# Performance work log

Hardware: AMD Instinct MI355X
Metric: run time of the kernel (lower is better)

The kernel has to match this reference:

```python
import jax, jax.numpy as jnp
import numpy as np

B, D, H = 8192, 256, 512


def setup_inputs() -> dict:
    key = jax.random.key(0)
    ks = jax.random.split(key, 25)
    inp = {
        "x": jax.random.normal(ks[0], (B, D), jnp.float32),
        "h_t": jax.random.normal(ks[1], (B, H), jnp.float32),
        "h_s": jax.random.normal(ks[2], (B, H), jnp.float32),
        "c_t": jax.random.normal(ks[3], (B, H), jnp.float32),
        "c_s": jax.random.normal(ks[4], (B, H), jnp.float32),
    }
    names = ["Ui", "Wti", "Wsi", "bi", "Us", "Wts", "Wss", "bs",
             "Ut", "Wtt", "Wst", "bt", "Uo", "Wto", "Wso", "bo",
             "Uc", "Wtc", "Wsc", "bc"]
    shapes = {"U": (D, H), "W": (H, H), "b": (H,)}
    scale = 0.02  # keep activations in a sane range
    for i, n in enumerate(names):
        s = shapes["U"] if n[0] == "U" else (shapes["b"] if n[0] == "b" else shapes["W"])
        inp[n] = jax.random.normal(ks[5 + i], s, jnp.float32) * scale
    return inp


def reference(x, h_t, h_s, c_t, c_s,
              Ui, Wti, Wsi, bi, Us, Wts, Wss, bs,
              Ut, Wtt, Wst, bt, Uo, Wto, Wso, bo,
              Uc, Wtc, Wsc, bc):
    # Fuse the 15 small GEMMs into 3 concatenated GEMMs: [B,D]@[D,5H] etc.
    U = jnp.concatenate([Ui, Us, Ut, Uo, Uc], axis=1)      # [D, 5H]
    Wt = jnp.concatenate([Wti, Wts, Wtt, Wto, Wtc], axis=1)  # [H, 5H]
    Ws = jnp.concatenate([Wsi, Wss, Wst, Wso, Wsc], axis=1)  # [H, 5H]
    b = jnp.concatenate([bi, bs, bt, bo, bc])                # [5H]
    gates = x @ U + h_t @ Wt + h_s @ Ws + b                  # [B, 5H]
    g_i, g_fs, g_ft, g_o, g_c = jnp.split(gates, 5, axis=1)
    i_n = jax.nn.sigmoid(g_i)
    f_s_n = jax.nn.sigmoid(g_fs)
    f_t_n = jax.nn.sigmoid(g_ft)
    o_n = jax.nn.sigmoid(g_o)
    c_n = jnp.tanh(g_c)
    c_h = i_n * c_n + f_t_n * c_t + f_s_n * c_s
    h = o_n * jnp.tanh(c_h)
    return (h, c_h)
```

## Files before the change

### kernel.cpp

```cpp
#include <hip/hip_runtime.h>
#include <hip/hip_bf16.h>
#include <cstdint>
#include <cstddef>

#define B_  8192
#define D_  256
#define H_  512
#define K_  1280
#define N_  2560
#define NT_ 160

typedef short short8 __attribute__((ext_vector_type(8)));
typedef float f32x4  __attribute__((ext_vector_type(4)));

__device__ __forceinline__ float sigf(float x)     { return 1.f / (1.f + __expf(-x)); }
__device__ __forceinline__ float tanhfast(float x) { return 1.f - 2.f / (__expf(2.f * x) + 1.f); }

__global__ void convA_kernel(const float* __restrict__ x, const float* __restrict__ ht,
                             const float* __restrict__ hs, __hip_bfloat16* __restrict__ A) {
    int t = blockIdx.x * 256 + threadIdx.x;
    int idx8 = t * 8;
    int b = idx8 / K_;
    int k = idx8 - b * K_;
    const float* src;
    if (k < D_)            src = x  + (size_t)b * D_ + k;
    else if (k < D_ + H_)  src = ht + (size_t)b * H_ + (k - D_);
    else                   src = hs + (size_t)b * H_ + (k - D_ - H_);
    f32x4 v0 = *(const f32x4*)(src);
    f32x4 v1 = *(const f32x4*)(src + 4);
    union { short8 s; __hip_bfloat16 h[8]; } o;
    o.h[0] = __float2bfloat16(v0[0]); o.h[1] = __float2bfloat16(v0[1]);
    o.h[2] = __float2bfloat16(v0[2]); o.h[3] = __float2bfloat16(v0[3]);
    o.h[4] = __float2bfloat16(v1[0]); o.h[5] = __float2bfloat16(v1[1]);
    o.h[6] = __float2bfloat16(v1[2]); o.h[7] = __float2bfloat16(v1[3]);
    *(short8*)(A + idx8) = o.s;
}

struct WPtrs {
    const float* U[5];
    const float* Wt[5];
    const float* Ws[5];
};

__global__ void convW_kernel(WPtrs p, __hip_bfloat16* __restrict__ WT) {
    __shared__ __hip_bfloat16 tile[64][72];
    int g  = blockIdx.z;
    int k0 = blockIdx.y * 64;
    int h0 = blockIdx.x * 64;
    const float* src; int kl0;
    if (k0 < 256)      { src = p.U[g];  kl0 = k0; }
    else if (k0 < 768) { src = p.Wt[g]; kl0 = k0 - 256; }
    else               { src = p.Ws[g]; kl0 = k0 - 768; }
    int tid = threadIdx.x;
    int tk = tid >> 6;
    int th = tid & 63;
    for (int r = 0; r < 16; ++r) {
        int kl = r * 4 + tk;
        tile[kl][th] = __float2bfloat16(src[(size_t)(kl0 + kl) * H_ + h0 + th]);
    }
    __syncthreads();
    for (int r = 0; r < 16; ++r) {
        int hl = r * 4 + tk;
        int h  = h0 + hl;
        int np = (h >> 4) * 80 + g * 16 + (h & 15);
        WT[(size_t)np * K_ + k0 + th] = tile[th][hl];
    }
}

#define GLD16(gp, lp)                                                              \
    __builtin_amdgcn_global_load_lds(                                              \
        (const __attribute__((address_space(1))) unsigned int*)(gp),               \
        (__attribute__((address_space(3))) unsigned int*)(lp), 16, 0, 0)

__global__ __launch_bounds__(256) void gemm_fused_kernel(
    const __hip_bfloat16* __restrict__ A, const __hip_bfloat16* __restrict__ WT,
    const float* __restrict__ ct, const float* __restrict__ cs,
    const float* __restrict__ bi, const float* __restrict__ bfs,
    const float* __restrict__ bft, const float* __restrict__ bo,
    const float* __restrict__ bc, float* __restrict__ out) {
    __shared__ alignas(16) unsigned short sA[128 * 32];
    __shared__ alignas(16) unsigned short sB[NT_ * 32];

    int tid = threadIdx.x;
    int m0 = blockIdx.y * 128;
    int n0 = blockIdx.x * NT_;
    int wid  = tid >> 6, lane = tid & 63;
    int wm   = wid >> 1, wn   = wid & 1;
    int quad = lane >> 4, l15 = lane & 15;

    int h = (blockIdx.x * 2 + wn) * 16 + l15;
    float Bi = bi[h], Bfs = bfs[h], Bft = bft[h], Bo = bo[h], Bc = bc[h];

    f32x4 acc[4][5];
    for (int i = 0; i < 4; ++i)
        for (int j = 0; j < 5; ++j)
            acc[i][j] = (f32x4){0.f, 0.f, 0.f, 0.f};

    int srow = tid >> 2;
    int scol = (tid & 3) * 8;
    const __hip_bfloat16* Abase = A  + (size_t)(m0 + srow) * K_ + scol;
    const __hip_bfloat16* Bbase = WT + (size_t)(n0 + srow) * K_ + scol;
    unsigned short* AsDst = sA + tid * 8;
    unsigned short* BsDst = sB + tid * 8;

    for (int k0 = 0; k0 < K_; k0 += 32) {
        GLD16(Abase + k0,                    AsDst);
        GLD16(Abase + k0 + (size_t)64 * K_,  AsDst + 2048);
        GLD16(Bbase + k0,                    BsDst);
        GLD16(Bbase + k0 + (size_t)64 * K_,  BsDst + 2048);
        if (tid < 128)
            GLD16(Bbase + k0 + (size_t)128 * K_, BsDst + 4096);
        __syncthreads();

        short8 a[4], b[5];
        for (int f = 0; f < 4; ++f)
            a[f] = *(const short8*)(sA + (wm * 64 + f * 16 + l15) * 32 + quad * 8);
        for (int j = 0; j < 5; ++j)
            b[j] = *(const short8*)(sB + (wn * 80 + j * 16 + l15) * 32 + quad * 8);
        for (int i = 0; i < 4; ++i)
            for (int j = 0; j < 5; ++j)
                acc[i][j] = __builtin_amdgcn_mfma_f32_16x16x32_bf16(a[i], b[j], acc[i][j], 0, 0, 0);
        __syncthreads();
    }

    for (int i = 0; i < 4; ++i) {
        int row0 = m0 + wm * 64 + i * 16 + quad * 4;
        for (int r = 0; r < 4; ++r) {
            size_t idx = (size_t)(row0 + r) * H_ + h;
            float i_n  = sigf(acc[i][0][r] + Bi);
            float fs_n = sigf(acc[i][1][r] + Bfs);
            float ft_n = sigf(acc[i][2][r] + Bft);
            float o_n  = sigf(acc[i][3][r] + Bo);
            float c_n  = tanhfast(acc[i][4][r] + Bc);
            float ch   = i_n * c_n + ft_n * ct[idx] + fs_n * cs[idx];
            out[idx] = o_n * tanhfast(ch);
            out[(size_t)B_ * H_ + idx] = ch;
        }
    }
}

struct AllW {
    const float* U[5];
    const float* Wt[5];
    const float* Ws[5];
    const float* bias[5];
};

__global__ __launch_bounds__(512) void fallback_kernel(const float* __restrict__ x,
                                                       const float* __restrict__ ht,
                                                       const float* __restrict__ hs,
                                                       const float* __restrict__ ct,
                                                       const float* __restrict__ cs,
                                                       AllW w, float* __restrict__ out) {
    __shared__ float arow[K_];
    int b = blockIdx.x;
    int h = threadIdx.x;
    for (int k = h; k < K_; k += 512) {
        float v;
        if (k < D_)           v = x[b * D_ + k];
        else if (k < D_ + H_) v = ht[b * H_ + k - D_];
        else                  v = hs[b * H_ + k - D_ - H_];
        arow[k] = v;
    }
    __syncthreads();
    float g[5];
    for (int gi = 0; gi < 5; ++gi) {
        float s = w.bias[gi][h];
        const float* U = w.U[gi];
        for (int k = 0; k < D_; ++k) s += arow[k] * U[(size_t)k * H_ + h];
        const float* Wt = w.Wt[gi];
        for (int k = 0; k < H_; ++k) s += arow[D_ + k] * Wt[(size_t)k * H_ + h];
        const float* Ws = w.Ws[gi];
        for (int k = 0; k < H_; ++k) s += arow[D_ + H_ + k] * Ws[(size_t)k * H_ + h];
        g[gi] = s;
    }
    int idx = b * H_ + h;
    float i_n = sigf(g[0]), fs_n = sigf(g[1]), ft_n = sigf(g[2]), o_n = sigf(g[3]);
    float c_n = tanhfast(g[4]);
    float ch  = i_n * c_n + ft_n * ct[idx] + fs_n * cs[idx];
    out[idx] = o_n * tanhfast(ch);
    out[(size_t)B_ * H_ + idx] = ch;
}

extern "C" void kernel_launch(void* const* d_in, const int* in_sizes, int n_in,
                              void* d_out, int out_size, void* d_ws, size_t ws_size,
                              hipStream_t stream) {
    const float* x  = (const float*)d_in[0];
    const float* ht = (const float*)d_in[1];
    const float* hs = (const float*)d_in[2];
    const float* ct = (const float*)d_in[3];
    const float* cs = (const float*)d_in[4];

    WPtrs wp;
    AllW  aw;
    const float* bias[5];
    for (int g = 0; g < 5; ++g) {
        wp.U[g]  = (const float*)d_in[5 + g * 4 + 0];
        wp.Wt[g] = (const float*)d_in[5 + g * 4 + 1];
        wp.Ws[g] = (const float*)d_in[5 + g * 4 + 2];
        bias[g]  = (const float*)d_in[5 + g * 4 + 3];
        aw.U[g] = wp.U[g]; aw.Wt[g] = wp.Wt[g]; aw.Ws[g] = wp.Ws[g]; aw.bias[g] = bias[g];
    }
    float* out = (float*)d_out;

    size_t szA = (size_t)B_ * K_ * 2;
    size_t szW = (size_t)N_ * K_ * 2;

    if (ws_size >= szA + szW) {
        __hip_bfloat16* Abf = (__hip_bfloat16*)d_ws;
        __hip_bfloat16* WT  = (__hip_bfloat16*)((char*)d_ws + szA);

        convA_kernel<<<(B_ * K_ / 8) / 256, 256, 0, stream>>>(x, ht, hs, Abf);
        convW_kernel<<<dim3(8, 20, 5), 256, 0, stream>>>(wp, WT);
        gemm_fused_kernel<<<dim3(N_ / NT_, B_ / 128), 256, 0, stream>>>(
            Abf, WT, ct, cs, bias[0], bias[1], bias[2], bias[3], bias[4], out);
    } else {
        fallback_kernel<<<B_, 512, 0, stream>>>(x, ht, hs, ct, cs, aw, out);
    }
}
```

Baseline: 248.2 us.

## Merge prep kernels and use 8-wave GEMM blocks with smaller per-wave tiles

The two conversion kernels become one launch, where a block-index range selects either activation conversion or weight transpose. The GEMM block grows from 4 to 8 waves, each computing a 32x80 tile instead of 64x80. This halves accumulator registers per wave and should allow more waves per CU for latency hiding. The grid is also transposed so that consecutive blocks walk along M, which changes L2 reuse of the weight tiles, and the loops are explicitly unrolled. In exchange, each wave does fewer MFMAs per LDS read of B, and each block now needs 512 threads to fill its tile.

```diff
diff --git a/kernel.cpp b/kernel.cpp
--- a/kernel.cpp
+++ b/kernel.cpp
@@ -16,54 +16,59 @@
 __device__ __forceinline__ float sigf(float x)     { return 1.f / (1.f + __expf(-x)); }
 __device__ __forceinline__ float tanhfast(float x) { return 1.f - 2.f / (__expf(2.f * x) + 1.f); }
 
-__global__ void convA_kernel(const float* __restrict__ x, const float* __restrict__ ht,
-                             const float* __restrict__ hs, __hip_bfloat16* __restrict__ A) {
-    int t = blockIdx.x * 256 + threadIdx.x;
-    int idx8 = t * 8;
-    int b = idx8 / K_;
-    int k = idx8 - b * K_;
-    const float* src;
-    if (k < D_)            src = x  + (size_t)b * D_ + k;
-    else if (k < D_ + H_)  src = ht + (size_t)b * H_ + (k - D_);
-    else                   src = hs + (size_t)b * H_ + (k - D_ - H_);
-    f32x4 v0 = *(const f32x4*)(src);
-    f32x4 v1 = *(const f32x4*)(src + 4);
-    union { short8 s; __hip_bfloat16 h[8]; } o;
-    o.h[0] = __float2bfloat16(v0[0]); o.h[1] = __float2bfloat16(v0[1]);
-    o.h[2] = __float2bfloat16(v0[2]); o.h[3] = __float2bfloat16(v0[3]);
-    o.h[4] = __float2bfloat16(v1[0]); o.h[5] = __float2bfloat16(v1[1]);
-    o.h[6] = __float2bfloat16(v1[2]); o.h[7] = __float2bfloat16(v1[3]);
-    *(short8*)(A + idx8) = o.s;
-}
-
 struct WPtrs {
     const float* U[5];
     const float* Wt[5];
     const float* Ws[5];
 };
 
-__global__ void convW_kernel(WPtrs p, __hip_bfloat16* __restrict__ WT) {
+__global__ void prep_kernel(const float* __restrict__ x, const float* __restrict__ ht,
+                            const float* __restrict__ hs, WPtrs p,
+                            __hip_bfloat16* __restrict__ A, __hip_bfloat16* __restrict__ WT) {
     __shared__ __hip_bfloat16 tile[64][72];
-    int g  = blockIdx.z;
-    int k0 = blockIdx.y * 64;
-    int h0 = blockIdx.x * 64;
-    const float* src; int kl0;
-    if (k0 < 256)      { src = p.U[g];  kl0 = k0; }
-    else if (k0 < 768) { src = p.Wt[g]; kl0 = k0 - 256; }
-    else               { src = p.Ws[g]; kl0 = k0 - 768; }
-    int tid = threadIdx.x;
-    int tk = tid >> 6;
-    int th = tid & 63;
-    for (int r = 0; r < 16; ++r) {
-        int kl = r * 4 + tk;
-        tile[kl][th] = __float2bfloat16(src[(size_t)(kl0 + kl) * H_ + h0 + th]);
-    }
-    __syncthreads();
-    for (int r = 0; r < 16; ++r) {
-        int hl = r * 4 + tk;
-        int h  = h0 + hl;
-        int np = (h >> 4) * 80 + g * 16 + (h & 15);
-        WT[(size_t)np * K_ + k0 + th] = tile[th][hl];
+    int bid = blockIdx.x;
+    if (bid < 5120) {
+        int t = bid * 256 + threadIdx.x;
+        int idx8 = t * 8;
+        int b = idx8 / K_;
+        int k = idx8 - b * K_;
+        const float* src;
+        if (k < D_)            src = x  + (size_t)b * D_ + k;
+        else if (k < D_ + H_)  src = ht + (size_t)b * H_ + (k - D_);
+        else                   src = hs + (size_t)b * H_ + (k - D_ - H_);
+        f32x4 v0 = *(const f32x4*)(src);
+        f32x4 v1 = *(const f32x4*)(src + 4);
+        union { short8 s; __hip_bfloat16 h[8]; } o;
+        o.h[0] = __float2bfloat16(v0[0]); o.h[1] = __float2bfloat16(v0[1]);
+        o.h[2] = __float2bfloat16(v0[2]); o.h[3] = __float2bfloat16(v0[3]);
+        o.h[4] = __float2bfloat16(v1[0]); o.h[5] = __float2bfloat16(v1[1]);
+        o.h[6] = __float2bfloat16(v1[2]); o.h[7] = __float2bfloat16(v1[3]);
+        *(short8*)(A + idx8) = o.s;
+    } else {
+        int bid2 = bid - 5120;
+        int hblk = bid2 & 7;
+        int kblk = (bid2 >> 3) % 20;
+        int g    = bid2 / 160;
+        int k0 = kblk * 64;
+        int h0 = hblk * 64;
+        const float* src; int kl0;
+        if (k0 < 256)      { src = p.U[g];  kl0 = k0; }
+        else if (k0 < 768) { src = p.Wt[g]; kl0 = k0 - 256; }
+        else               { src = p.Ws[g]; kl0 = k0 - 768; }
+        int tid = threadIdx.x;
+        int tk = tid >> 6;
+        int th = tid & 63;
+        for (int r = 0; r < 16; ++r) {
+            int kl = r * 4 + tk;
+            tile[kl][th] = __float2bfloat16(src[(size_t)(kl0 + kl) * H_ + h0 + th]);
+        }
+        __syncthreads();
+        for (int r = 0; r < 16; ++r) {
+            int hl = r * 4 + tk;
+            int h  = h0 + hl;
+            int np = (h >> 4) * 80 + g * 16 + (h & 15);
+            WT[(size_t)np * K_ + k0 + th] = tile[th][hl];
+        }
     }
 }
 
@@ -72,7 +77,7 @@
         (const __attribute__((address_space(1))) unsigned int*)(gp),               \
         (__attribute__((address_space(3))) unsigned int*)(lp), 16, 0, 0)
 
-__global__ __launch_bounds__(256) void gemm_fused_kernel(
+__global__ __launch_bounds__(512, 4) void gemm_fused_kernel(
     const __hip_bfloat16* __restrict__ A, const __hip_bfloat16* __restrict__ WT,
     const float* __restrict__ ct, const float* __restrict__ cs,
     const float* __restrict__ bi, const float* __restrict__ bfs,
@@ -82,17 +87,20 @@
     __shared__ alignas(16) unsigned short sB[NT_ * 32];
 
     int tid = threadIdx.x;
-    int m0 = blockIdx.y * 128;
-    int n0 = blockIdx.x * NT_;
+    int m0 = blockIdx.x * 128;
+    int n0 = blockIdx.y * NT_;
     int wid  = tid >> 6, lane = tid & 63;
-    int wm   = wid >> 1, wn   = wid & 1;
+    int wm   = wid >> 1;
+    int wn   = wid & 1;
     int quad = lane >> 4, l15 = lane & 15;
 
-    int h = (blockIdx.x * 2 + wn) * 16 + l15;
+    int h = (blockIdx.y * 2 + wn) * 16 + l15;
     float Bi = bi[h], Bfs = bfs[h], Bft = bft[h], Bo = bo[h], Bc = bc[h];
 
-    f32x4 acc[4][5];
-    for (int i = 0; i < 4; ++i)
+    f32x4 acc[2][5];
+#pragma unroll
+    for (int i = 0; i < 2; ++i)
+#pragma unroll
         for (int j = 0; j < 5; ++j)
             acc[i][j] = (f32x4){0.f, 0.f, 0.f, 0.f};
 
@@ -104,27 +112,31 @@
     unsigned short* BsDst = sB + tid * 8;
 
     for (int k0 = 0; k0 < K_; k0 += 32) {
-        GLD16(Abase + k0,                    AsDst);
-        GLD16(Abase + k0 + (size_t)64 * K_,  AsDst + 2048);
-        GLD16(Bbase + k0,                    BsDst);
-        GLD16(Bbase + k0 + (size_t)64 * K_,  BsDst + 2048);
+        GLD16(Abase + k0, AsDst);
+        GLD16(Bbase + k0, BsDst);
         if (tid < 128)
             GLD16(Bbase + k0 + (size_t)128 * K_, BsDst + 4096);
         __syncthreads();
 
-        short8 a[4], b[5];
-        for (int f = 0; f < 4; ++f)
-            a[f] = *(const short8*)(sA + (wm * 64 + f * 16 + l15) * 32 + quad * 8);
+        short8 a[2], b[5];
+#pragma unroll
+        for (int i = 0; i < 2; ++i)
+            a[i] = *(const short8*)(sA + (wm * 32 + i * 16 + l15) * 32 + quad * 8);
+#pragma unroll
         for (int j = 0; j < 5; ++j)
             b[j] = *(const short8*)(sB + (wn * 80 + j * 16 + l15) * 32 + quad * 8);
-        for (int i = 0; i < 4; ++i)
-            for (int j = 0; j < 5; ++j)
+#pragma unroll
+        for (int j = 0; j < 5; ++j)
+#pragma unroll
+            for (int i = 0; i < 2; ++i)
                 acc[i][j] = __builtin_amdgcn_mfma_f32_16x16x32_bf16(a[i], b[j], acc[i][j], 0, 0, 0);
         __syncthreads();
     }
 
-    for (int i = 0; i < 4; ++i) {
-        int row0 = m0 + wm * 64 + i * 16 + quad * 4;
+#pragma unroll
+    for (int i = 0; i < 2; ++i) {
+        int row0 = m0 + wm * 32 + i * 16 + quad * 4;
+#pragma unroll
         for (int r = 0; r < 4; ++r) {
             size_t idx = (size_t)(row0 + r) * H_ + h;
             float i_n  = sigf(acc[i][0][r] + Bi);
@@ -210,9 +222,8 @@
         __hip_bfloat16* Abf = (__hip_bfloat16*)d_ws;
         __hip_bfloat16* WT  = (__hip_bfloat16*)((char*)d_ws + szA);
 
-        convA_kernel<<<(B_ * K_ / 8) / 256, 256, 0, stream>>>(x, ht, hs, Abf);
-        convW_kernel<<<dim3(8, 20, 5), 256, 0, stream>>>(wp, WT);
-        gemm_fused_kernel<<<dim3(N_ / NT_, B_ / 128), 256, 0, stream>>>(
+        prep_kernel<<<5120 + 800, 256, 0, stream>>>(x, ht, hs, wp, Abf, WT);
+        gemm_fused_kernel<<<dim3(B_ / 128, N_ / NT_), 512, 0, stream>>>(
             Abf, WT, ct, cs, bias[0], bias[1], bias[2], bias[3], bias[4], out);
     } else {
         fallback_kernel<<<B_, 512, 0, stream>>>(x, ht, hs, ct, cs, aw, out);
```

Result: faster. 242.6 us (-2.3%).
